# Kernel tuning notes

Measured on AMD Instinct MI355X. Metric: run time of the kernel, lower is better.

## Reference

```python
import jax, jax.numpy as jnp
import numpy as np

B, L, S, H, E = 2, 2048, 2048, 8, 64

def setup_inputs() -> dict:
    key = jax.random.key(0)
    k1, k2, k3 = jax.random.split(key, 3)
    queries = jax.random.normal(k1, (B, L, H, E), dtype=jnp.float32)
    keys = jax.random.normal(k2, (B, S, H, E), dtype=jnp.float32)
    values = jax.random.normal(k3, (B, S, H, E), dtype=jnp.float32)
    # TriangularCausalMask: True above the diagonal (positions to mask out)
    attn_mask = jnp.broadcast_to(
        jnp.triu(jnp.ones((L, S), dtype=bool), k=1)[None, None], (B, 1, L, S)
    )
    return {"queries": queries, "keys": keys, "values": values, "attn_mask": attn_mask}

def reference(queries, keys, values, attn_mask):
    E_ = queries.shape[-1]
    scale = 1.0 / (E_ ** 0.5)  # self.scale is None -> 1/sqrt(E)
    # scores: [B, H, L, S]
    scores = jnp.einsum('blhe,bshe->bhls', queries, keys)
    scores = jnp.where(attn_mask, -jnp.inf, scores)  # masked_fill_(mask, -inf)
    series = jax.nn.softmax(scale * scores, axis=-1)  # dropout p=0.0 -> identity
    V = jnp.einsum('bhls,bshd->blhd', series, values)
    return V, series
```

## Files before the change

### kernel.cpp

```cpp
#include <hip/hip_runtime.h>
#include <hip/hip_bf16.h>

typedef __attribute__((ext_vector_type(8))) short bf16x8;
typedef __attribute__((ext_vector_type(4))) float f32x4;

constexpr int B = 2, L = 2048, S = 2048, H = 8, E = 64;
constexpr int TL = 64;
constexpr int SN = 64;
constexpr int LDK = 72;
constexpr int THREADS = 256;

__device__ __forceinline__ short f2bf(float x) {
  union { float f; unsigned u; } c; c.f = x;
  unsigned r = c.u + 0x7fffu + ((c.u >> 16) & 1u);
  return (short)(r >> 16);
}
__device__ __forceinline__ float bf2f(short s) {
  union { unsigned u; float f; } c; c.u = ((unsigned)(unsigned short)s) << 16;
  return c.f;
}

__device__ __forceinline__ void ld16(const float* __restrict__ p, short* __restrict__ t) {
  const float4* q = (const float4*)p;
  float4 v0 = q[0], v1 = q[1], v2 = q[2], v3 = q[3];
  float vv[16] = { v0.x,v0.y,v0.z,v0.w, v1.x,v1.y,v1.z,v1.w,
                   v2.x,v2.y,v2.z,v2.w, v3.x,v3.y,v3.z,v3.w };
#pragma unroll
  for (int k = 0; k < 8; ++k) {
    __hip_bfloat162 h = __float22bfloat162_rn(make_float2(vv[2*k], vv[2*k+1]));
    short2 s2 = *(short2*)&h;
    t[2*k] = s2.x; t[2*k+1] = s2.y;
  }
}

__device__ __forceinline__ void stage64(const float* __restrict__ g,
                                        short (* __restrict__ lds)[LDK],
                                        int tid, size_t gstride) {
  const int r = tid >> 2, c = (tid & 3) * 16;
  short t[16];
  ld16(g + (size_t)r * gstride + c, t);
  *(bf16x8*)&lds[r][c]     = *(bf16x8*)&t[0];
  *(bf16x8*)&lds[r][c + 8] = *(bf16x8*)&t[8];
}

__device__ __forceinline__ void stageVt(const float* __restrict__ g,
                                        short (* __restrict__ Vt)[LDK],
                                        int tid, size_t gstride) {
  const int s = tid >> 2, c = (tid & 3) * 16;
  short t[16];
  ld16(g + (size_t)s * gstride + c, t);
#pragma unroll
  for (int i = 0; i < 16; ++i) {
    const int e = c + i;
    Vt[e][s ^ (8 * ((e >> 3) & 7))] = t[i];
  }
}

__global__ __launch_bounds__(THREADS, 2)
void attn_tile(const float* __restrict__ Q, const float* __restrict__ K,
               const float* __restrict__ V, float* __restrict__ outV,
               float* __restrict__ outS)
{
  __shared__ __align__(16) short Qs[TL][LDK];
  __shared__ __align__(16) short Ks[SN][LDK];
  __shared__ __align__(16) short Vt[E][LDK];
  __shared__ __align__(16) short Ps[4][16][LDK];
  __shared__ float inv_lds[TL];

  const int tid  = threadIdx.x;
  const int lane = tid & 63;
  const int wv   = tid >> 6;
  const int quad = lane >> 4;
  const int n16  = lane & 15;

  int t = blockIdx.x;
  t = (t & 1) ? (31 - (t >> 1)) : (t >> 1);
  const int bh = blockIdx.y;
  const int b = bh >> 3, h = bh & 7;
  const int l0 = t * TL;
  const int s_hi = l0 + TL;
  const int nt = s_hi / SN;

  const size_t gstr  = (size_t)H * E;
  const size_t qbase = ((size_t)b * L * H + h) * E;
  const size_t kbase = ((size_t)b * S * H + h) * E;
  const size_t srow  = (size_t)bh * L * S;

  {
    const float4 z = make_float4(0.f, 0.f, 0.f, 0.f);
    for (int r = 0; r < TL; ++r) {
      float4* p = (float4*)(outS + srow + (size_t)(l0 + r) * S);
      for (int s4 = s_hi / 4 + tid; s4 < S / 4; s4 += THREADS)
        p[s4] = z;
    }
  }

  stage64(Q + qbase + (size_t)l0 * gstr, Qs, tid, gstr);
  __syncthreads();

  float rsum[4] = {0.f, 0.f, 0.f, 0.f};
  for (int st = 0; st < nt; ++st) {
    const int s0 = st * SN;
    __syncthreads();
    stage64(K + kbase + (size_t)s0 * gstr, Ks, tid, gstr);
    __syncthreads();

    bf16x8 a0 = *(const bf16x8*)&Qs[wv * 16 + n16][quad * 8];
    bf16x8 a1 = *(const bf16x8*)&Qs[wv * 16 + n16][32 + quad * 8];
#pragma unroll
    for (int nn = 0; nn < 4; ++nn) {
      bf16x8 b0 = *(const bf16x8*)&Ks[nn * 16 + n16][quad * 8];
      bf16x8 b1 = *(const bf16x8*)&Ks[nn * 16 + n16][32 + quad * 8];
      f32x4 acc = {0.f, 0.f, 0.f, 0.f};
      acc = __builtin_amdgcn_mfma_f32_16x16x32_bf16(a0, b0, acc, 0, 0, 0);
      acc = __builtin_amdgcn_mfma_f32_16x16x32_bf16(a1, b1, acc, 0, 0, 0);
#pragma unroll
      for (int r = 0; r < 4; ++r) {
        const int l = l0 + wv * 16 + quad * 4 + r;
        const int s = s0 + nn * 16 + n16;
        rsum[r] += (s <= l) ? __expf(acc[r] * 0.125f) : 0.f;
      }
    }
  }
#pragma unroll
  for (int r = 0; r < 4; ++r)
#pragma unroll
    for (int off = 1; off < 16; off <<= 1)
      rsum[r] += __shfl_xor(rsum[r], off, 64);
  if (n16 == 0)
#pragma unroll
    for (int r = 0; r < 4; ++r)
      inv_lds[wv * 16 + quad * 4 + r] = 1.f / rsum[r];
  __syncthreads();

  float inv_r[4];
#pragma unroll
  for (int r = 0; r < 4; ++r) inv_r[r] = inv_lds[wv * 16 + quad * 4 + r];

  f32x4 oacc[4] = {{0,0,0,0},{0,0,0,0},{0,0,0,0},{0,0,0,0}};
  for (int st = 0; st < nt; ++st) {
    const int s0 = st * SN;
    __syncthreads();
    stage64(K + kbase + (size_t)s0 * gstr, Ks, tid, gstr);
    stageVt(V + kbase + (size_t)s0 * gstr, Vt, tid, gstr);
    __syncthreads();

    bf16x8 a0 = *(const bf16x8*)&Qs[wv * 16 + n16][quad * 8];
    bf16x8 a1 = *(const bf16x8*)&Qs[wv * 16 + n16][32 + quad * 8];
#pragma unroll
    for (int nn = 0; nn < 4; ++nn) {
      bf16x8 b0 = *(const bf16x8*)&Ks[nn * 16 + n16][quad * 8];
      bf16x8 b1 = *(const bf16x8*)&Ks[nn * 16 + n16][32 + quad * 8];
      f32x4 acc = {0.f, 0.f, 0.f, 0.f};
      acc = __builtin_amdgcn_mfma_f32_16x16x32_bf16(a0, b0, acc, 0, 0, 0);
      acc = __builtin_amdgcn_mfma_f32_16x16x32_bf16(a1, b1, acc, 0, 0, 0);
#pragma unroll
      for (int r = 0; r < 4; ++r) {
        const int l = l0 + wv * 16 + quad * 4 + r;
        const int s = s0 + nn * 16 + n16;
        float w = (s <= l) ? __expf(acc[r] * 0.125f) * inv_r[r] : 0.f;
        Ps[wv][quad * 4 + r][(nn * 16 + n16) ^ (8 * quad)] = f2bf(w);
      }
    }
    __syncthreads();

    {
      const int psw = 8 * ((n16 >> 2) & 3);
      bf16x8 p0 = *(const bf16x8*)&Ps[wv][n16][(quad * 16)     ^ psw];
      bf16x8 p1 = *(const bf16x8*)&Ps[wv][n16][(quad * 16 + 8) ^ psw];
      float4 o0 = make_float4(bf2f(p0[0]), bf2f(p0[1]), bf2f(p0[2]), bf2f(p0[3]));
      float4 o1 = make_float4(bf2f(p0[4]), bf2f(p0[5]), bf2f(p0[6]), bf2f(p0[7]));
      float4 o2 = make_float4(bf2f(p1[0]), bf2f(p1[1]), bf2f(p1[2]), bf2f(p1[3]));
      float4 o3 = make_float4(bf2f(p1[4]), bf2f(p1[5]), bf2f(p1[6]), bf2f(p1[7]));
      float4* dst = (float4*)(outS + srow + (size_t)(l0 + wv * 16 + n16) * S + s0 + quad * 16);
      dst[0] = o0; dst[1] = o1; dst[2] = o2; dst[3] = o3;
    }

    {
      const int psw = 8 * ((n16 >> 2) & 3);
      bf16x8 pa0 = *(const bf16x8*)&Ps[wv][n16][(quad * 8)      ^ psw];
      bf16x8 pa1 = *(const bf16x8*)&Ps[wv][n16][(32 + quad * 8) ^ psw];
#pragma unroll
      for (int nn = 0; nn < 4; ++nn) {
        const int e   = nn * 16 + n16;
        const int vsw = 8 * ((e >> 3) & 7);
        bf16x8 vb0 = *(const bf16x8*)&Vt[e][(quad * 8)      ^ vsw];
        bf16x8 vb1 = *(const bf16x8*)&Vt[e][(32 + quad * 8) ^ vsw];
        oacc[nn] = __builtin_amdgcn_mfma_f32_16x16x32_bf16(pa0, vb0, oacc[nn], 0, 0, 0);
        oacc[nn] = __builtin_amdgcn_mfma_f32_16x16x32_bf16(pa1, vb1, oacc[nn], 0, 0, 0);
      }
    }
  }

#pragma unroll
  for (int nn = 0; nn < 4; ++nn)
#pragma unroll
    for (int r = 0; r < 4; ++r) {
      const int l = l0 + wv * 16 + quad * 4 + r;
      outV[qbase + (size_t)l * gstr + nn * 16 + n16] = oacc[nn][r];
    }
}

extern "C" void kernel_launch(void* const* d_in, const int* in_sizes, int n_in,
                              void* d_out, int out_size, void* d_ws, size_t ws_size,
                              hipStream_t stream) {
  const float* Q = (const float*)d_in[0];
  const float* K = (const float*)d_in[1];
  const float* V = (const float*)d_in[2];
  float* outV = (float*)d_out;
  float* outS = outV + (size_t)B * L * H * E;
  attn_tile<<<dim3(L / TL, B * H), THREADS, 0, stream>>>(Q, K, V, outV, outS);
}
```

Measured before the change: 409.0 us.

## Fuse two-pass softmax into single pass with deferred row rescale kernel

Replaces the two passes over K (one for row sums, one for probabilities and PV) with a single pass that writes unnormalized exp scores and accumulates unnormalized output, then normalizes the output in registers. A second kernel rescales every score row by the stored inverse sum and zero-fills the masked region, which moves the zero-fill out of the main kernel. K/V global loads are prefetched into registers one tile ahead to overlap with compute. This removes one QK^T pass and the repeated K loads, but adds a full read-modify-write pass over the L×S score matrix. Scores are still rounded to bf16 before normalization, and rows are not max-subtracted, so exp could overflow for large logits.

```diff
diff --git a/kernel.cpp b/kernel.cpp
--- a/kernel.cpp
+++ b/kernel.cpp
@@ -20,52 +20,25 @@
   return c.f;
 }
 
-__device__ __forceinline__ void ld16(const float* __restrict__ p, short* __restrict__ t) {
-  const float4* q = (const float4*)p;
-  float4 v0 = q[0], v1 = q[1], v2 = q[2], v3 = q[3];
-  float vv[16] = { v0.x,v0.y,v0.z,v0.w, v1.x,v1.y,v1.z,v1.w,
-                   v2.x,v2.y,v2.z,v2.w, v3.x,v3.y,v3.z,v3.w };
+__device__ __forceinline__ void cvt16(const float4* v, short* t) {
+  const float* f = (const float*)v;
 #pragma unroll
   for (int k = 0; k < 8; ++k) {
-    __hip_bfloat162 h = __float22bfloat162_rn(make_float2(vv[2*k], vv[2*k+1]));
+    __hip_bfloat162 h = __float22bfloat162_rn(make_float2(f[2*k], f[2*k+1]));
     short2 s2 = *(short2*)&h;
     t[2*k] = s2.x; t[2*k+1] = s2.y;
   }
 }
 
-__device__ __forceinline__ void stage64(const float* __restrict__ g,
-                                        short (* __restrict__ lds)[LDK],
-                                        int tid, size_t gstride) {
-  const int r = tid >> 2, c = (tid & 3) * 16;
-  short t[16];
-  ld16(g + (size_t)r * gstride + c, t);
-  *(bf16x8*)&lds[r][c]     = *(bf16x8*)&t[0];
-  *(bf16x8*)&lds[r][c + 8] = *(bf16x8*)&t[8];
-}
-
-__device__ __forceinline__ void stageVt(const float* __restrict__ g,
-                                        short (* __restrict__ Vt)[LDK],
-                                        int tid, size_t gstride) {
-  const int s = tid >> 2, c = (tid & 3) * 16;
-  short t[16];
-  ld16(g + (size_t)s * gstride + c, t);
-#pragma unroll
-  for (int i = 0; i < 16; ++i) {
-    const int e = c + i;
-    Vt[e][s ^ (8 * ((e >> 3) & 7))] = t[i];
-  }
-}
-
 __global__ __launch_bounds__(THREADS, 2)
-void attn_tile(const float* __restrict__ Q, const float* __restrict__ K,
-               const float* __restrict__ V, float* __restrict__ outV,
-               float* __restrict__ outS)
+void attn_fused(const float* __restrict__ Q, const float* __restrict__ K,
+                const float* __restrict__ V, float* __restrict__ outV,
+                float* __restrict__ outS, float* __restrict__ ws)
 {
   __shared__ __align__(16) short Qs[TL][LDK];
   __shared__ __align__(16) short Ks[SN][LDK];
   __shared__ __align__(16) short Vt[E][LDK];
   __shared__ __align__(16) short Ps[4][16][LDK];
-  __shared__ float inv_lds[TL];
 
   const int tid  = threadIdx.x;
   const int lane = tid & 63;
@@ -78,8 +51,7 @@
   const int bh = blockIdx.y;
   const int b = bh >> 3, h = bh & 7;
   const int l0 = t * TL;
-  const int s_hi = l0 + TL;
-  const int nt = s_hi / SN;
+  const int nt = (l0 + TL) / SN;
 
   const size_t gstr  = (size_t)H * E;
   const size_t qbase = ((size_t)b * L * H + h) * E;
@@ -87,26 +59,49 @@
   const size_t srow  = (size_t)bh * L * S;
 
   {
-    const float4 z = make_float4(0.f, 0.f, 0.f, 0.f);
-    for (int r = 0; r < TL; ++r) {
-      float4* p = (float4*)(outS + srow + (size_t)(l0 + r) * S);
-      for (int s4 = s_hi / 4 + tid; s4 < S / 4; s4 += THREADS)
-        p[s4] = z;
-    }
-  }
-
-  stage64(Q + qbase + (size_t)l0 * gstr, Qs, tid, gstr);
+    const int r = tid >> 2, c = (tid & 3) * 16;
+    float4 q4[4];
+    const float4* p = (const float4*)(Q + qbase + (size_t)(l0 + r) * gstr + c);
+    q4[0] = p[0]; q4[1] = p[1]; q4[2] = p[2]; q4[3] = p[3];
+    short tq[16]; cvt16(q4, tq);
+    *(bf16x8*)&Qs[r][c]     = *(bf16x8*)&tq[0];
+    *(bf16x8*)&Qs[r][c + 8] = *(bf16x8*)&tq[8];
+  }
+
+  const int sr = tid >> 2, scol = (tid & 3) * 16;
+  float4 kr[4], vr[4];
+  auto ldKV = [&](int s0) {
+    const float4* kp = (const float4*)(K + kbase + (size_t)(s0 + sr) * gstr + scol);
+    kr[0] = kp[0]; kr[1] = kp[1]; kr[2] = kp[2]; kr[3] = kp[3];
+    const float4* vp = (const float4*)(V + kbase + (size_t)(s0 + sr) * gstr + scol);
+    vr[0] = vp[0]; vr[1] = vp[1]; vr[2] = vp[2]; vr[3] = vp[3];
+  };
+  auto writeKV = [&]() {
+    short tk[16]; cvt16(kr, tk);
+    *(bf16x8*)&Ks[sr][scol]     = *(bf16x8*)&tk[0];
+    *(bf16x8*)&Ks[sr][scol + 8] = *(bf16x8*)&tk[8];
+    short tv[16]; cvt16(vr, tv);
+#pragma unroll
+    for (int i = 0; i < 16; ++i) {
+      const int e = scol + i;
+      Vt[e][sr ^ (8 * ((e >> 3) & 7))] = tv[i];
+    }
+  };
+
+  ldKV(0);
+  writeKV();
   __syncthreads();
 
+  bf16x8 a0 = *(const bf16x8*)&Qs[wv * 16 + n16][quad * 8];
+  bf16x8 a1 = *(const bf16x8*)&Qs[wv * 16 + n16][32 + quad * 8];
+
   float rsum[4] = {0.f, 0.f, 0.f, 0.f};
+  f32x4 oacc[4] = {{0,0,0,0},{0,0,0,0},{0,0,0,0},{0,0,0,0}};
+
   for (int st = 0; st < nt; ++st) {
     const int s0 = st * SN;
-    __syncthreads();
-    stage64(K + kbase + (size_t)s0 * gstr, Ks, tid, gstr);
-    __syncthreads();
-
-    bf16x8 a0 = *(const bf16x8*)&Qs[wv * 16 + n16][quad * 8];
-    bf16x8 a1 = *(const bf16x8*)&Qs[wv * 16 + n16][32 + quad * 8];
+    if (st + 1 < nt) ldKV(s0 + SN);
+
 #pragma unroll
     for (int nn = 0; nn < 4; ++nn) {
       bf16x8 b0 = *(const bf16x8*)&Ks[nn * 16 + n16][quad * 8];
@@ -118,54 +113,15 @@
       for (int r = 0; r < 4; ++r) {
         const int l = l0 + wv * 16 + quad * 4 + r;
         const int s = s0 + nn * 16 + n16;
-        rsum[r] += (s <= l) ? __expf(acc[r] * 0.125f) : 0.f;
-      }
-    }
-  }
-#pragma unroll
-  for (int r = 0; r < 4; ++r)
-#pragma unroll
-    for (int off = 1; off < 16; off <<= 1)
-      rsum[r] += __shfl_xor(rsum[r], off, 64);
-  if (n16 == 0)
-#pragma unroll
-    for (int r = 0; r < 4; ++r)
-      inv_lds[wv * 16 + quad * 4 + r] = 1.f / rsum[r];
-  __syncthreads();
-
-  float inv_r[4];
-#pragma unroll
-  for (int r = 0; r < 4; ++r) inv_r[r] = inv_lds[wv * 16 + quad * 4 + r];
-
-  f32x4 oacc[4] = {{0,0,0,0},{0,0,0,0},{0,0,0,0},{0,0,0,0}};
-  for (int st = 0; st < nt; ++st) {
-    const int s0 = st * SN;
-    __syncthreads();
-    stage64(K + kbase + (size_t)s0 * gstr, Ks, tid, gstr);
-    stageVt(V + kbase + (size_t)s0 * gstr, Vt, tid, gstr);
-    __syncthreads();
-
-    bf16x8 a0 = *(const bf16x8*)&Qs[wv * 16 + n16][quad * 8];
-    bf16x8 a1 = *(const bf16x8*)&Qs[wv * 16 + n16][32 + quad * 8];
-#pragma unroll
-    for (int nn = 0; nn < 4; ++nn) {
-      bf16x8 b0 = *(const bf16x8*)&Ks[nn * 16 + n16][quad * 8];
-      bf16x8 b1 = *(const bf16x8*)&Ks[nn * 16 + n16][32 + quad * 8];
-      f32x4 acc = {0.f, 0.f, 0.f, 0.f};
-      acc = __builtin_amdgcn_mfma_f32_16x16x32_bf16(a0, b0, acc, 0, 0, 0);
-      acc = __builtin_amdgcn_mfma_f32_16x16x32_bf16(a1, b1, acc, 0, 0, 0);
-#pragma unroll
-      for (int r = 0; r < 4; ++r) {
-        const int l = l0 + wv * 16 + quad * 4 + r;
-        const int s = s0 + nn * 16 + n16;
-        float w = (s <= l) ? __expf(acc[r] * 0.125f) * inv_r[r] : 0.f;
+        float w = (s <= l) ? __expf(acc[r] * 0.125f) : 0.f;
+        rsum[r] += w;
         Ps[wv][quad * 4 + r][(nn * 16 + n16) ^ (8 * quad)] = f2bf(w);
       }
     }
     __syncthreads();
 
     {
-      const int psw = 8 * ((n16 >> 2) & 3);
+      const int psw = 8 * (n16 >> 2);
       bf16x8 p0 = *(const bf16x8*)&Ps[wv][n16][(quad * 16)     ^ psw];
       bf16x8 p1 = *(const bf16x8*)&Ps[wv][n16][(quad * 16 + 8) ^ psw];
       float4 o0 = make_float4(bf2f(p0[0]), bf2f(p0[1]), bf2f(p0[2]), bf2f(p0[3]));
@@ -177,7 +133,7 @@
     }
 
     {
-      const int psw = 8 * ((n16 >> 2) & 3);
+      const int psw = 8 * (n16 >> 2);
       bf16x8 pa0 = *(const bf16x8*)&Ps[wv][n16][(quad * 8)      ^ psw];
       bf16x8 pa1 = *(const bf16x8*)&Ps[wv][n16][(32 + quad * 8) ^ psw];
 #pragma unroll
@@ -190,15 +146,63 @@
         oacc[nn] = __builtin_amdgcn_mfma_f32_16x16x32_bf16(pa1, vb1, oacc[nn], 0, 0, 0);
       }
     }
-  }
+
+    if (st + 1 < nt) {
+      __syncthreads();
+      writeKV();
+      __syncthreads();
+    }
+  }
+
+#pragma unroll
+  for (int r = 0; r < 4; ++r)
+#pragma unroll
+    for (int off = 1; off < 16; off <<= 1)
+      rsum[r] += __shfl_xor(rsum[r], off, 64);
+  float inv_r[4];
+#pragma unroll
+  for (int r = 0; r < 4; ++r) inv_r[r] = 1.f / rsum[r];
+  if (n16 == 0)
+#pragma unroll
+    for (int r = 0; r < 4; ++r)
+      ws[(size_t)bh * L + l0 + wv * 16 + quad * 4 + r] = inv_r[r];
 
 #pragma unroll
   for (int nn = 0; nn < 4; ++nn)
 #pragma unroll
     for (int r = 0; r < 4; ++r) {
       const int l = l0 + wv * 16 + quad * 4 + r;
-      outV[qbase + (size_t)l * gstr + nn * 16 + n16] = oacc[nn][r];
-    }
+      outV[qbase + (size_t)l * gstr + nn * 16 + n16] = oacc[nn][r] * inv_r[r];
+    }
+}
+
+__global__ __launch_bounds__(THREADS)
+void rescale_rows(const float* __restrict__ ws, float* __restrict__ outS)
+{
+  const int row = blockIdx.x;
+  const int l   = row & (L - 1);
+  const float inv = ws[row];
+  float4* p = (float4*)(outS + (size_t)row * S);
+  const float4 z = make_float4(0.f, 0.f, 0.f, 0.f);
+#pragma unroll
+  for (int it = 0; it < S / 4 / THREADS; ++it) {
+    const int s4 = threadIdx.x + it * THREADS;
+    const int sb = s4 * 4;
+    if (sb + 3 <= l) {
+      float4 v = p[s4];
+      v.x *= inv; v.y *= inv; v.z *= inv; v.w *= inv;
+      p[s4] = v;
+    } else if (sb > l) {
+      p[s4] = z;
+    } else {
+      float4 v = p[s4];
+      v.x = (sb + 0 <= l) ? v.x * inv : 0.f;
+      v.y = (sb + 1 <= l) ? v.y * inv : 0.f;
+      v.z = (sb + 2 <= l) ? v.z * inv : 0.f;
+      v.w = (sb + 3 <= l) ? v.w * inv : 0.f;
+      p[s4] = v;
+    }
+  }
 }
 
 extern "C" void kernel_launch(void* const* d_in, const int* in_sizes, int n_in,
@@ -209,5 +213,7 @@
   const float* V = (const float*)d_in[2];
   float* outV = (float*)d_out;
   float* outS = outV + (size_t)B * L * H * E;
-  attn_tile<<<dim3(L / TL, B * H), THREADS, 0, stream>>>(Q, K, V, outV, outS);
-}
+  float* ws   = (float*)d_ws;
+  attn_fused<<<dim3(L / TL, B * H), THREADS, 0, stream>>>(Q, K, V, outV, outS, ws);
+  rescale_rows<<<dim3(B * H * L), THREADS, 0, stream>>>(ws, outS);
+}
```

Result: slower. 421.2 us (+3.0%).
